# Optimization experiments

Measured on AMD Instinct MI355X. Metric: run time of the kernel, lower is better.

Reference implementation:

```python
import jax, jax.numpy as jnp
import numpy as np

NH, NOPE_D, ROPE_D, V_D, R = 16, 48, 16, 64, 128
EPS = 1e-6

def rms_norm(x, w):
    norm = jax.lax.rsqrt(jnp.mean(jnp.square(x), axis=-1, keepdims=True) + EPS)
    return x * norm * w

def apply_rope(x, cos, sin):
    # x: (..., rope_d); cos/sin broadcastable (..., rope_d//2)
    d = x.shape[-1]
    x1, x2 = x[..., : d // 2], x[..., d // 2 :]
    return jnp.concatenate([x1 * cos - x2 * sin, x2 * cos + x1 * sin], axis=-1)

def setup_inputs() -> dict:
    key = jax.random.key(0)
    ks = jax.random.split(key, 8)
    B, T, D = 2, 2048, 1024
    s = lambda fan_in: 1.0 / np.sqrt(fan_in)
    return {
        "x": jax.random.normal(ks[0], (B, T, D), jnp.float32),
        "cos": jax.random.uniform(ks[1], (T, ROPE_D // 2), jnp.float32),
        "sin": jax.random.uniform(ks[2], (T, ROPE_D // 2), jnp.float32),
        "Wq": jax.random.normal(ks[3], (NH * (NOPE_D + ROPE_D), D), jnp.float32) * s(D),
        "q_norm_w": jnp.ones((NOPE_D + ROPE_D,), jnp.float32),
        "Wkva": jax.random.normal(ks[4], (R + ROPE_D, D), jnp.float32) * s(D),
        "kva_norm_w": jnp.ones((R,), jnp.float32),
        "Wkvb": jax.random.normal(ks[5], (NH * (NOPE_D + V_D), R), jnp.float32) * s(R),
        "Wo": jax.random.normal(ks[6], (D, NH * V_D), jnp.float32) * s(NH * V_D),
    }

def reference(x, cos, sin, Wq, q_norm_w, Wkva, kva_norm_w, Wkvb, Wo):
    B, T, D = x.shape
    # Q path: project, per-head RMSNorm over (nope+rope) dims, split
    q = (x @ Wq.T).reshape(B, T, NH, NOPE_D + ROPE_D)
    q = rms_norm(q, q_norm_w)
    q_nope, q_rope = q[..., :NOPE_D], q[..., NOPE_D:]
    # Low-rank KV path
    kv_a = x @ Wkva.T  # (B,T,R+ROPE_D)
    kv_latent = rms_norm(kv_a[..., :R], kva_norm_w)
    k_rope_raw = kv_a[..., R:]  # (B,T,ROPE_D) shared across heads
    kv_b = (kv_latent @ Wkvb.T).reshape(B, T, NH, NOPE_D + V_D)
    k_nope, v = kv_b[..., :NOPE_D], kv_b[..., NOPE_D:]
    # Decoupled RoPE
    cos_t = cos[None, :T, None, :]  # (1,T,1,rope_d/2)
    sin_t = sin[None, :T, None, :]
    q_rope = apply_rope(q_rope, cos_t, sin_t)
    k_rope = apply_rope(k_rope_raw[:, :, None, :], cos[None, :T, None, :], sin[None, :T, None, :])
    k_rope = jnp.broadcast_to(k_rope, (B, T, NH, ROPE_D))
    q_full = jnp.concatenate([q_nope, q_rope], axis=-1)  # (B,T,NH,64)
    k_full = jnp.concatenate([k_nope, k_rope], axis=-1)
    # Causal attention, scale = 1/sqrt(nope+rope)
    scale = (NOPE_D + ROPE_D) ** -0.5
    scores = jnp.einsum("bqhd,bkhd->bhqk", q_full, k_full) * scale
    causal = jnp.tril(jnp.ones((T, T), bool))
    scores = jnp.where(causal[None, None], scores, -jnp.inf)
    attn = jax.nn.softmax(scores, axis=-1)
    out = jnp.einsum("bhqk,bkhd->bqhd", attn, v).reshape(B, T, NH * V_D)
    return out @ Wo.T
```

## Files before the change

### kernel.cpp

```cpp
#include <hip/hip_runtime.h>
#include <hip/hip_bf16.h>
#include <math.h>

#define NH 16
#define T_ 2048
#define B_ 2
#define D_ 1024
#define EPS 1e-6f

typedef __attribute__((ext_vector_type(8))) short bf16x8;
typedef __attribute__((ext_vector_type(4))) float f32x4;

__device__ __forceinline__ float wred_sum(float v){
  #pragma unroll
  for (int o = 32; o > 0; o >>= 1) v += __shfl_xor(v, o, 64);
  return v;
}

__device__ __forceinline__ unsigned pack_bf16(float a, float b){
  __hip_bfloat162 t = __float22bfloat162_rn(make_float2(a, b));
  unsigned r; __builtin_memcpy(&r, &t, 4); return r;
}

__device__ __forceinline__ void gload_lds16(const void* g, void* l){
  __builtin_amdgcn_global_load_lds((const __attribute__((address_space(1))) void*)g,
                                   (__attribute__((address_space(3))) void*)l, 16, 0, 0);
}

__global__ __launch_bounds__(256)
void cvt5(const float* __restrict__ x, const float* __restrict__ wq,
          const float* __restrict__ wkva, const float* __restrict__ wkvb,
          const float* __restrict__ wo,
          __hip_bfloat16* __restrict__ xb, __hip_bfloat16* __restrict__ wqb,
          __hip_bfloat16* __restrict__ wkvab, __hip_bfloat16* __restrict__ wkvbb,
          __hip_bfloat16* __restrict__ wob)
{
  const int i = blockIdx.x * 256 + threadIdx.x;
  const float* s; __hip_bfloat16* d; size_t soff, doff;
  if      (i < 1048576) { s = x;    d = xb;    soff = doff = i; }
  else if (i < 1310720) { s = wq;   d = wqb;   soff = doff = i - 1048576; }
  else if (i < 1347584) { s = wkva; d = wkvab; soff = doff = i - 1310720; }
  else if (i < 1404928) {
    const int off = i - 1347584;
    const int srow = off >> 5, c4 = off & 31;
    const int h = srow / 112, dd = srow % 112;
    const int drow = (dd < 48) ? (h*48 + dd) : (768 + h*64 + (dd - 48));
    s = wkvb; d = wkvbb; soff = off; doff = (size_t)drow*32 + c4;
  }
  else                  { s = wo;   d = wob;   soff = doff = i - 1404928; }
  float4 v = *(const float4*)(s + soff * 4);
  *(__hip_bfloat162*)(d + doff * 4)     = __float22bfloat162_rn(make_float2(v.x, v.y));
  *(__hip_bfloat162*)(d + doff * 4 + 2) = __float22bfloat162_rn(make_float2(v.z, v.w));
}

template<typename CT>
__global__ __launch_bounds__(256, 2)
void gemm_bt64(const __hip_bfloat16* __restrict__ A, const __hip_bfloat16* __restrict__ W,
               CT* __restrict__ C, int M, int N, int K)
{
  __shared__ __hip_bfloat16 As[2][128 * 64];
  __shared__ __hip_bfloat16 Ws[2][64 * 64];
  const int tid = threadIdx.x;
  const int wv = tid >> 6, lane = tid & 63;
  const int m = lane & 15, quad = lane >> 4;
  const int bm = blockIdx.y * 128, bn = blockIdx.x * 64;

  const __hip_bfloat16* ga[4];
  const __hip_bfloat16* gw[2];
  #pragma unroll
  for (int i = 0; i < 4; i++) {
    const int slot = i*256 + tid;
    const int row = slot >> 3, cb = slot & 7;
    ga[i] = A + (size_t)(bm + row) * K + ((cb ^ (row & 7)) << 3);
  }
  #pragma unroll
  for (int i = 0; i < 2; i++) {
    const int slot = i*256 + tid;
    const int row = slot >> 3, cb = slot & 7;
    int wr = bn + row; if (wr >= N) wr = N - 1;
    gw[i] = W + (size_t)wr * K + ((cb ^ (row & 7)) << 3);
  }
  auto stage = [&](int buf){
    #pragma unroll
    for (int i = 0; i < 4; i++) { gload_lds16(ga[i], &As[buf][(i*256 + wv*64)*8]); ga[i] += 64; }
    #pragma unroll
    for (int i = 0; i < 2; i++) { gload_lds16(gw[i], &Ws[buf][(i*256 + wv*64)*8]); gw[i] += 64; }
  };

  f32x4 acc[2][4];
  #pragma unroll
  for (int mi = 0; mi < 2; mi++)
    #pragma unroll
    for (int nj = 0; nj < 4; nj++) acc[mi][nj] = (f32x4){0.f,0.f,0.f,0.f};

  stage(0);
  const int iters = K >> 6;
  for (int it = 0; it < iters; it++) {
    const int cur = it & 1;
    __syncthreads();
    if (it + 1 < iters) stage(cur ^ 1);
    #pragma unroll
    for (int ks = 0; ks < 2; ks++) {
      const int cb = ((ks*4 + quad) ^ (m & 7)) << 3;
      bf16x8 af[2], wf[4];
      #pragma unroll
      for (int mi = 0; mi < 2; mi++)
        af[mi] = *(const bf16x8*)(&As[cur][(wv*32 + mi*16 + m) * 64 + cb]);
      #pragma unroll
      for (int nj = 0; nj < 4; nj++)
        wf[nj] = *(const bf16x8*)(&Ws[cur][(nj*16 + m) * 64 + cb]);
      #pragma unroll
      for (int mi = 0; mi < 2; mi++)
        #pragma unroll
        for (int nj = 0; nj < 4; nj++)
          acc[mi][nj] = __builtin_amdgcn_mfma_f32_16x16x32_bf16(af[mi], wf[nj], acc[mi][nj], 0, 0, 0);
    }
  }

  #pragma unroll
  for (int mi = 0; mi < 2; mi++)
    #pragma unroll
    for (int nj = 0; nj < 4; nj++) {
      const int col = bn + nj*16 + m;
      if (col < N) {
        #pragma unroll
        for (int r = 0; r < 4; r++) {
          const int row = bm + wv*32 + mi*16 + quad*4 + r;
          if constexpr (sizeof(CT) == 2)
            C[(size_t)row * N + col] = (CT)__float2bfloat16(acc[mi][nj][r]);
          else
            C[(size_t)row * N + col] = acc[mi][nj][r];
        }
      }
    }
}

__global__ __launch_bounds__(256, 2)
void gemm_qkva(const __hip_bfloat16* __restrict__ A, const __hip_bfloat16* __restrict__ Wqb,
               const __hip_bfloat16* __restrict__ Wkvab,
               const float* __restrict__ qw, const float* __restrict__ cosp,
               const float* __restrict__ sinp,
               __hip_bfloat16* __restrict__ qb, float* __restrict__ kva)
{
  __shared__ __hip_bfloat16 As[2][128 * 64];
  __shared__ __hip_bfloat16 Ws[2][64 * 64];
  const int K = 1024;
  const int tid = threadIdx.x;
  const int wv = tid >> 6, lane = tid & 63;
  const int m = lane & 15, quad = lane >> 4;
  const int bm = blockIdx.y * 128;
  const bool isq = blockIdx.x < 16;
  const __hip_bfloat16* W = isq ? Wqb : Wkvab;
  const int bn = isq ? blockIdx.x*64 : (blockIdx.x - 16)*64;
  const int Nw = isq ? 1024 : 144;

  const __hip_bfloat16* ga[4];
  const __hip_bfloat16* gw[2];
  #pragma unroll
  for (int i = 0; i < 4; i++) {
    const int slot = i*256 + tid;
    const int row = slot >> 3, cb = slot & 7;
    ga[i] = A + (size_t)(bm + row) * K + ((cb ^ (row & 7)) << 3);
  }
  #pragma unroll
  for (int i = 0; i < 2; i++) {
    const int slot = i*256 + tid;
    const int row = slot >> 3, cb = slot & 7;
    int wr = bn + row; if (wr >= Nw) wr = Nw - 1;
    gw[i] = W + (size_t)wr * K + ((cb ^ (row & 7)) << 3);
  }
  auto stage = [&](int buf){
    #pragma unroll
    for (int i = 0; i < 4; i++) { gload_lds16(ga[i], &As[buf][(i*256 + wv*64)*8]); ga[i] += 64; }
    #pragma unroll
    for (int i = 0; i < 2; i++) { gload_lds16(gw[i], &Ws[buf][(i*256 + wv*64)*8]); gw[i] += 64; }
  };

  f32x4 acc[2][4];
  #pragma unroll
  for (int mi = 0; mi < 2; mi++)
    #pragma unroll
    for (int nj = 0; nj < 4; nj++) acc[mi][nj] = (f32x4){0.f,0.f,0.f,0.f};

  stage(0);
  for (int it = 0; it < 16; it++) {
    const int cur = it & 1;
    __syncthreads();
    if (it < 15) stage(cur ^ 1);
    #pragma unroll
    for (int ks = 0; ks < 2; ks++) {
      const int cb = ((ks*4 + quad) ^ (m & 7)) << 3;
      bf16x8 af[2], wf[4];
      #pragma unroll
      for (int mi = 0; mi < 2; mi++)
        af[mi] = *(const bf16x8*)(&As[cur][(wv*32 + mi*16 + m) * 64 + cb]);
      #pragma unroll
      for (int nj = 0; nj < 4; nj++)
        wf[nj] = *(const bf16x8*)(&Ws[cur][(nj*16 + m) * 64 + cb]);
      #pragma unroll
      for (int mi = 0; mi < 2; mi++)
        #pragma unroll
        for (int nj = 0; nj < 4; nj++)
          acc[mi][nj] = __builtin_amdgcn_mfma_f32_16x16x32_bf16(af[mi], wf[nj], acc[mi][nj], 0, 0, 0);
    }
  }

  if (isq) {
    const int head = blockIdx.x;
    float qwv[4];
    #pragma unroll
    for (int nj = 0; nj < 4; nj++) qwv[nj] = qw[nj*16 + m];
    const int j = m & 7;
    const float qscale = 0.125f * 1.44269504f;
    #pragma unroll
    for (int mi = 0; mi < 2; mi++) {
      #pragma unroll
      for (int r = 0; r < 4; r++) {
        float ss = 0.f;
        #pragma unroll
        for (int nj = 0; nj < 4; nj++) { const float t = acc[mi][nj][r]; ss = fmaf(t, t, ss); }
        ss += __shfl_xor(ss, 1, 64); ss += __shfl_xor(ss, 2, 64);
        ss += __shfl_xor(ss, 4, 64); ss += __shfl_xor(ss, 8, 64);
        const float nrm = rsqrtf(ss * (1.0f/64.0f) + EPS);
        float v[4];
        #pragma unroll
        for (int nj = 0; nj < 4; nj++) v[nj] = acc[mi][nj][r] * nrm * qwv[nj];
        const int grow = bm + wv*32 + mi*16 + quad*4 + r;
        const int t = grow & (T_ - 1);
        const int b = grow >> 11;
        const float part = __shfl_xor(v[3], 8, 64);
        const float c = cosp[t*8 + j], sn = sinp[t*8 + j];
        v[3] = (m < 8) ? (v[3]*c - part*sn) : (v[3]*c + part*sn);
        __hip_bfloat16* dst = qb + ((size_t)(b*NH + head)*T_ + t)*64 + m;
        #pragma unroll
        for (int nj = 0; nj < 4; nj++) dst[nj*16] = __float2bfloat16(v[nj] * qscale);
      }
    }
  } else {
    #pragma unroll
    for (int mi = 0; mi < 2; mi++)
      #pragma unroll
      for (int nj = 0; nj < 4; nj++) {
        const int col = bn + nj*16 + m;
        if (col < 144) {
          #pragma unroll
          for (int r = 0; r < 4; r++) {
            const int row = bm + wv*32 + mi*16 + quad*4 + r;
            kva[(size_t)row * 144 + col] = acc[mi][nj][r];
          }
        }
      }
  }
}

__global__ void prep_kv(const float* __restrict__ kva, const float* __restrict__ kw,
                        const float* __restrict__ cosp, const float* __restrict__ sinp,
                        __hip_bfloat16* __restrict__ kvl16, __hip_bfloat16* __restrict__ krope16)
{
  const int tid = threadIdx.x;
  const int bt = blockIdx.x;
  const int t = bt % T_;
  const float* row = kva + (size_t)bt * 144;
  const float v = row[tid];
  float s = wred_sum(v * v);
  __shared__ float red[2];
  if ((tid & 63) == 0) red[tid >> 6] = s;
  __syncthreads();
  const float total = red[0] + red[1];
  const float norm = rsqrtf(total * (1.0f/128.0f) + EPS);
  kvl16[(size_t)bt * 128 + tid] = __float2bfloat16(v * norm * kw[tid]);
  if (tid < 16) {
    const int j = tid & 7;
    const float c = cosp[t*8 + j], sn = sinp[t*8 + j];
    const float x1 = row[128 + j], x2 = row[136 + j];
    krope16[(size_t)bt * 16 + tid] = __float2bfloat16((tid < 8) ? (x1 * c - x2 * sn)
                                                               : (x2 * c + x1 * sn));
  }
}

__global__ __launch_bounds__(256, 2)
void gemm_kvb(const __hip_bfloat16* __restrict__ A, const __hip_bfloat16* __restrict__ W,
              __hip_bfloat16* __restrict__ knope, __hip_bfloat16* __restrict__ vt)
{
  __shared__ __hip_bfloat16 As[2][128 * 64];
  __shared__ __hip_bfloat16 Ws[2][64 * 64];
  const int K = 128;
  const int tid = threadIdx.x;
  const int wv = tid >> 6, lane = tid & 63;
  const int m = lane & 15, quad = lane >> 4;
  const int bm = blockIdx.y * 128, bn = blockIdx.x * 64;

  const __hip_bfloat16* ga[4];
  const __hip_bfloat16* gw[2];
  #pragma unroll
  for (int i = 0; i < 4; i++) {
    const int slot = i*256 + tid;
    const int row = slot >> 3, cb = slot & 7;
    ga[i] = A + (size_t)(bm + row) * K + ((cb ^ (row & 7)) << 3);
  }
  #pragma unroll
  for (int i = 0; i < 2; i++) {
    const int slot = i*256 + tid;
    const int row = slot >> 3, cb = slot & 7;
    gw[i] = W + (size_t)(bn + row) * K + ((cb ^ (row & 7)) << 3);
  }
  auto stage = [&](int buf){
    #pragma unroll
    for (int i = 0; i < 4; i++) { gload_lds16(ga[i], &As[buf][(i*256 + wv*64)*8]); ga[i] += 64; }
    #pragma unroll
    for (int i = 0; i < 2; i++) { gload_lds16(gw[i], &Ws[buf][(i*256 + wv*64)*8]); gw[i] += 64; }
  };

  f32x4 acc[2][4];
  #pragma unroll
  for (int mi = 0; mi < 2; mi++)
    #pragma unroll
    for (int nj = 0; nj < 4; nj++) acc[mi][nj] = (f32x4){0.f,0.f,0.f,0.f};

  stage(0);
  for (int it = 0; it < 2; it++) {
    const int cur = it & 1;
    __syncthreads();
    if (it == 0) stage(1);
    #pragma unroll
    for (int ks = 0; ks < 2; ks++) {
      const int cb = ((ks*4 + quad) ^ (m & 7)) << 3;
      bf16x8 af[2], wf[4];
      #pragma unroll
      for (int mi = 0; mi < 2; mi++)
        af[mi] = *(const bf16x8*)(&As[cur][(wv*32 + mi*16 + m) * 64 + cb]);
      #pragma unroll
      for (int nj = 0; nj < 4; nj++)
        wf[nj] = *(const bf16x8*)(&Ws[cur][(nj*16 + m) * 64 + cb]);
      #pragma unroll
      for (int mi = 0; mi < 2; mi++)
        #pragma unroll
        for (int nj = 0; nj < 4; nj++)
          acc[mi][nj] = __builtin_amdgcn_mfma_f32_16x16x32_bf16(af[mi], wf[nj], acc[mi][nj], 0, 0, 0);
    }
  }

  if (bn < 768) {
    #pragma unroll
    for (int mi = 0; mi < 2; mi++)
      #pragma unroll
      for (int nj = 0; nj < 4; nj++) {
        const int col = bn + nj*16 + m;
        #pragma unroll
        for (int r = 0; r < 4; r++) {
          const int row = bm + wv*32 + mi*16 + quad*4 + r;
          knope[(size_t)row * 768 + col] = __float2bfloat16(acc[mi][nj][r]);
        }
      }
  } else {
    __syncthreads();
    short* TL = (short*)&As[0][0];
    #pragma unroll
    for (int mi = 0; mi < 2; mi++)
      #pragma unroll
      for (int nj = 0; nj < 4; nj++) {
        const int d = nj*16 + m;
        #pragma unroll
        for (int r = 0; r < 4; r++) {
          const int tl = wv*32 + mi*16 + quad*4 + r;
          __hip_bfloat16 hv = __float2bfloat16(acc[mi][nj][r]);
          short sv; __builtin_memcpy(&sv, &hv, 2);
          TL[d*136 + tl] = sv;
        }
      }
    __syncthreads();
    const int h = (bn - 768) >> 6;
    const int b = bm >> 11;
    const int t0 = bm & (T_ - 1);
    #pragma unroll
    for (int i = 0; i < 4; i++) {
      const int unit = i*256 + tid;
      const int d = unit >> 4, tu = unit & 15;
      *(bf16x8*)(vt + ((size_t)(b*NH + h)*64 + d)*T_ + t0 + tu*8)
          = *(const bf16x8*)(TL + d*136 + tu*8);
    }
  }
}

__device__ __forceinline__ void fa_softmax_fixed(f32x4 (&s)[8], const bool diag,
    const int k0, const int qglob, const int m, const int quad,
    float& lrun, bf16x8 (&a)[4])
{
  if (diag) {
    #pragma unroll
    for (int sub = 0; sub < 8; sub++)
      #pragma unroll
      for (int r = 0; r < 4; r++)
        if (k0 + sub*16 + quad*4 + r > qglob) s[sub][r] = -1e30f;
  }
  float p[8][4];
  #pragma unroll
  for (int sub = 0; sub < 8; sub++)
    #pragma unroll
    for (int r = 0; r < 4; r++) {
      const float e = exp2f(s[sub][r] - 48.0f);
      p[sub][r] = e; lrun += e;
    }

  unsigned u[8][2];
  #pragma unroll
  for (int sub = 0; sub < 8; sub++) {
    u[sub][0] = pack_bf16(p[sub][0], p[sub][1]);
    u[sub][1] = pack_bf16(p[sub][2], p[sub][3]);
  }
  #pragma unroll
  for (int c = 0; c < 4; c++) {
    union { int i[4]; bf16x8 v; } au;
    #pragma unroll
    for (int w4 = 0; w4 < 4; w4++) {
      const int src = (((2*quad + (w4 >> 1)) & 3) << 4) | m;
      const int lo = __shfl((int)u[c*2][w4 & 1], src, 64);
      const int hi = __shfl((int)u[c*2+1][w4 & 1], src, 64);
      au.i[w4] = (quad & 2) ? hi : lo;
    }
    a[c] = au.v;
  }
}

__device__ __forceinline__ void fa_store(float lrun, f32x4 (&oacc)[4],
    const int b, const int qrow0, const int h, const int m, const int quad,
    __hip_bfloat16* __restrict__ aout)
{
  lrun += __shfl_xor(lrun, 16, 64);
  lrun += __shfl_xor(lrun, 32, 64);
  float lr[4];
  #pragma unroll
  for (int r = 0; r < 4; r++) lr[r] = __shfl(lrun, (quad << 2) | r, 64);
  #pragma unroll
  for (int vs = 0; vs < 4; vs++)
    #pragma unroll
    for (int r = 0; r < 4; r++)
      aout[(size_t)(b*T_ + qrow0 + quad*4 + r) * 1024 + h*64 + vs*16 + m]
          = __float2bfloat16(oacc[vs][r] / lr[r]);
}

__global__ __launch_bounds__(256, 2)
void attn_pair2(const __hip_bfloat16* __restrict__ qb,
                const __hip_bfloat16* __restrict__ knope,
                const __hip_bfloat16* __restrict__ krope16,
                const __hip_bfloat16* __restrict__ vt16,
                __hip_bfloat16* __restrict__ aout)
{
  __shared__ __hip_bfloat16 SL[32768];
  const int tid = threadIdx.x;
  const int wv = tid >> 6, lane = tid & 63;
  const int m = lane & 15, quad = lane >> 4;
  const int ta = blockIdx.x;
  const int tb = 31 - ta;
  const int bh = blockIdx.y;
  const int b = bh >> 4, h = bh & 15;
  const int qbaseA = ta*64 + wv*16;
  const int qbaseB = tb*64 + wv*16;
  const int ntA = (ta + 2) >> 1;
  const int ntB = (tb + 2) >> 1;

  const __hip_bfloat16* qra = qb + ((size_t)bh*T_ + qbaseA + m)*64 + quad*8;
  const bf16x8 qA0 = *(const bf16x8*)qra, qA1 = *(const bf16x8*)(qra + 32);
  const __hip_bfloat16* qrb = qb + ((size_t)bh*T_ + qbaseB + m)*64 + quad*8;
  const bf16x8 qB0 = *(const bf16x8*)qrb, qB1 = *(const bf16x8*)(qrb + 32);

  const __hip_bfloat16* pK[4]; size_t iK[4];
  const __hip_bfloat16* pV[4];
  #pragma unroll
  for (int i = 0; i < 4; i++) {
    const int slot = i*256 + tid;
    const int krow = slot >> 3;
    const int kde = (slot & 7) ^ (krow & 7);
    if (kde < 6) { pK[i] = knope + (size_t)(b*T_ + krow)*768 + h*48 + kde*8; iK[i] = (size_t)128*768; }
    else         { pK[i] = krope16 + (size_t)(b*T_ + krow)*16 + (kde-6)*8;   iK[i] = (size_t)128*16; }
    const int vd = slot >> 4;
    const int vde = (slot & 15) ^ (vd & 7);
    pV[i] = vt16 + ((size_t)bh*64 + vd)*T_ + vde*8;
  }

  auto stage = [&](int buf){
    #pragma unroll
    for (int i = 0; i < 4; i++) {
      gload_lds16(pK[i], SL + buf*8192 + (i*256 + wv*64)*8);
      gload_lds16(pV[i], SL + 16384 + buf*8192 + (i*256 + wv*64)*8);
      pK[i] += iK[i]; pV[i] += 128;
    }
  };

  f32x4 oA[4], oB[4];
  #pragma unroll
  for (int vs = 0; vs < 4; vs++) { oA[vs] = (f32x4){0.f,0.f,0.f,0.f}; oB[vs] = (f32x4){0.f,0.f,0.f,0.f}; }
  float lA = 0.f, lB = 0.f;

  const int sw0 = quad ^ (m & 7);
  stage(0);

  for (int kt = 0; kt < ntB; kt++) {
    const int cur = kt & 1;
    __syncthreads();
    const __hip_bfloat16* Kc = SL + cur*8192;
    const __hip_bfloat16* Vc = SL + 16384 + cur*8192;
    const bool doA = (kt < ntA);

    f32x4 sA[8], sB[8];
    #pragma unroll
    for (int sub = 0; sub < 8; sub++) {
      const bf16x8 kf0 = *(const bf16x8*)(Kc + (sub*16 + m)*64 + sw0*8);
      const bf16x8 kf1 = *(const bf16x8*)(Kc + (sub*16 + m)*64 + (sw0^4)*8);
      f32x4 z = (f32x4){0.f,0.f,0.f,0.f};
      z = __builtin_amdgcn_mfma_f32_16x16x32_bf16(kf0, qB0, z, 0, 0, 0);
      z = __builtin_amdgcn_mfma_f32_16x16x32_bf16(kf1, qB1, z, 0, 0, 0);
      sB[sub] = z;
      if (doA) {
        f32x4 y = (f32x4){0.f,0.f,0.f,0.f};
        y = __builtin_amdgcn_mfma_f32_16x16x32_bf16(kf0, qA0, y, 0, 0, 0);
        y = __builtin_amdgcn_mfma_f32_16x16x32_bf16(kf1, qA1, y, 0, 0, 0);
        sA[sub] = y;
      }
    }

    if (kt + 1 < ntB) stage(cur ^ 1);

    bf16x8 aA[4], aB[4];
    fa_softmax_fixed(sB, kt == ntB-1, kt*128, qbaseB + m, m, quad, lB, aB);
    if (doA) fa_softmax_fixed(sA, kt == ntA-1, kt*128, qbaseA + m, m, quad, lA, aA);

    #pragma unroll
    for (int vs = 0; vs < 4; vs++) {
      #pragma unroll
      for (int c = 0; c < 4; c++) {
        const bf16x8 vf = *(const bf16x8*)(Vc + (vs*16 + m)*128 + (((c*4 + quad) ^ (m & 7)) << 3));
        oB[vs] = __builtin_amdgcn_mfma_f32_16x16x32_bf16(aB[c], vf, oB[vs], 0, 0, 0);
        if (doA) oA[vs] = __builtin_amdgcn_mfma_f32_16x16x32_bf16(aA[c], vf, oA[vs], 0, 0, 0);
      }
    }
  }

  fa_store(lA, oA, b, qbaseA, h, m, quad, aout);
  fa_store(lB, oB, b, qbaseB, h, m, quad, aout);
}

extern "C" void kernel_launch(void* const* d_in, const int* in_sizes, int n_in,
                              void* d_out, int out_size, void* d_ws, size_t ws_size,
                              hipStream_t stream)
{
  const float* x    = (const float*)d_in[0];
  const float* cosp = (const float*)d_in[1];
  const float* sinp = (const float*)d_in[2];
  const float* Wq   = (const float*)d_in[3];
  const float* qw   = (const float*)d_in[4];
  const float* Wkva = (const float*)d_in[5];
  const float* kw   = (const float*)d_in[6];
  const float* Wkvb = (const float*)d_in[7];
  const float* Wo   = (const float*)d_in[8];
  float* out = (float*)d_out;

  float* kva = (float*)d_ws;
  __hip_bfloat16* xb16    = (__hip_bfloat16*)(kva + 589824);
  __hip_bfloat16* knope16 = xb16 + 4194304;
  __hip_bfloat16* kvl16   = knope16 + 3145728;
  __hip_bfloat16* qb16    = kvl16 + 524288;
  __hip_bfloat16* vt16    = qb16 + 4194304;
  __hip_bfloat16* krope16 = vt16 + 4194304;
  __hip_bfloat16* Wqb     = krope16 + 65536;
  __hip_bfloat16* Wkvab   = Wqb + 1048576;
  __hip_bfloat16* Wkvbb   = Wkvab + 147456;
  __hip_bfloat16* Wob     = Wkvbb + 229376;
  __hip_bfloat16* ab16    = Wob + 1048576;

  const int M = B_ * T_;

  cvt5<<<6512, 256, 0, stream>>>(x, Wq, Wkva, Wkvb, Wo, xb16, Wqb, Wkvab, Wkvbb, Wob);
  gemm_qkva<<<dim3(19, 32), 256, 0, stream>>>(xb16, Wqb, Wkvab, qw, cosp, sinp, qb16, kva);
  prep_kv<<<M, 128, 0, stream>>>(kva, kw, cosp, sinp, kvl16, krope16);
  gemm_kvb<<<dim3(28, 32), 256, 0, stream>>>(kvl16, Wkvbb, knope16, vt16);
  attn_pair2<<<dim3(16, B_ * NH), 256, 0, stream>>>(qb16, knope16, krope16, vt16, ab16);
  gemm_bt64<float><<<dim3(16, 32), 256, 0, stream>>>(ab16, Wob, out, M, 1024, 1024);
}
```

Baseline: 185.1 us.

## Replace paired-tile attention with single 64-key tiles and diagonal skip

The attention kernel no longer pairs two 64-row query tiles per block over 128-key steps. It now gives each block one query tile and walks 64-key tiles, skipping the masked QK MFMAs on the diagonal tile. Blocks are permuted across query tiles to balance the causal load, and LDS is halved so four blocks can fit per CU. The cost is that K/V are no longer shared between two query tiles, and there are twice as many blocks and barriers per key.

```diff
diff --git a/kernel.cpp b/kernel.cpp
--- a/kernel.cpp
+++ b/kernel.cpp
@@ -382,46 +382,6 @@
   }
 }
 
-__device__ __forceinline__ void fa_softmax_fixed(f32x4 (&s)[8], const bool diag,
-    const int k0, const int qglob, const int m, const int quad,
-    float& lrun, bf16x8 (&a)[4])
-{
-  if (diag) {
-    #pragma unroll
-    for (int sub = 0; sub < 8; sub++)
-      #pragma unroll
-      for (int r = 0; r < 4; r++)
-        if (k0 + sub*16 + quad*4 + r > qglob) s[sub][r] = -1e30f;
-  }
-  float p[8][4];
-  #pragma unroll
-  for (int sub = 0; sub < 8; sub++)
-    #pragma unroll
-    for (int r = 0; r < 4; r++) {
-      const float e = exp2f(s[sub][r] - 48.0f);
-      p[sub][r] = e; lrun += e;
-    }
-
-  unsigned u[8][2];
-  #pragma unroll
-  for (int sub = 0; sub < 8; sub++) {
-    u[sub][0] = pack_bf16(p[sub][0], p[sub][1]);
-    u[sub][1] = pack_bf16(p[sub][2], p[sub][3]);
-  }
-  #pragma unroll
-  for (int c = 0; c < 4; c++) {
-    union { int i[4]; bf16x8 v; } au;
-    #pragma unroll
-    for (int w4 = 0; w4 < 4; w4++) {
-      const int src = (((2*quad + (w4 >> 1)) & 3) << 4) | m;
-      const int lo = __shfl((int)u[c*2][w4 & 1], src, 64);
-      const int hi = __shfl((int)u[c*2+1][w4 & 1], src, 64);
-      au.i[w4] = (quad & 2) ? hi : lo;
-    }
-    a[c] = au.v;
-  }
-}
-
 __device__ __forceinline__ void fa_store(float lrun, f32x4 (&oacc)[4],
     const int b, const int qrow0, const int h, const int m, const int quad,
     __hip_bfloat16* __restrict__ aout)
@@ -439,105 +399,131 @@
           = __float2bfloat16(oacc[vs][r] / lr[r]);
 }
 
-__global__ __launch_bounds__(256, 2)
-void attn_pair2(const __hip_bfloat16* __restrict__ qb,
-                const __hip_bfloat16* __restrict__ knope,
-                const __hip_bfloat16* __restrict__ krope16,
-                const __hip_bfloat16* __restrict__ vt16,
-                __hip_bfloat16* __restrict__ aout)
-{
-  __shared__ __hip_bfloat16 SL[32768];
+__global__ __launch_bounds__(256, 4)
+void attn_tile(const __hip_bfloat16* __restrict__ qb,
+               const __hip_bfloat16* __restrict__ knope,
+               const __hip_bfloat16* __restrict__ krope16,
+               const __hip_bfloat16* __restrict__ vt16,
+               __hip_bfloat16* __restrict__ aout)
+{
+  __shared__ __hip_bfloat16 SL[16384];
   const int tid = threadIdx.x;
   const int wv = tid >> 6, lane = tid & 63;
   const int m = lane & 15, quad = lane >> 4;
-  const int ta = blockIdx.x;
-  const int tb = 31 - ta;
+  const int idx = (blockIdx.x + blockIdx.y) & 31;
+  const int pj = idx & 7, pk = idx >> 3;
+  const int qt = (pk == 0) ? pj : (pk == 1) ? (15 - pj) : (pk == 2) ? (16 + pj) : (31 - pj);
   const int bh = blockIdx.y;
   const int b = bh >> 4, h = bh & 15;
-  const int qbaseA = ta*64 + wv*16;
-  const int qbaseB = tb*64 + wv*16;
-  const int ntA = (ta + 2) >> 1;
-  const int ntB = (tb + 2) >> 1;
-
-  const __hip_bfloat16* qra = qb + ((size_t)bh*T_ + qbaseA + m)*64 + quad*8;
-  const bf16x8 qA0 = *(const bf16x8*)qra, qA1 = *(const bf16x8*)(qra + 32);
-  const __hip_bfloat16* qrb = qb + ((size_t)bh*T_ + qbaseB + m)*64 + quad*8;
-  const bf16x8 qB0 = *(const bf16x8*)qrb, qB1 = *(const bf16x8*)(qrb + 32);
-
-  const __hip_bfloat16* pK[4]; size_t iK[4];
-  const __hip_bfloat16* pV[4];
-  #pragma unroll
-  for (int i = 0; i < 4; i++) {
+  const int qbase = qt*64 + wv*16;
+  const int nt = qt + 1;
+
+  const __hip_bfloat16* qr = qb + ((size_t)bh*T_ + qbase + m)*64 + quad*8;
+  const bf16x8 q0 = *(const bf16x8*)qr, q1 = *(const bf16x8*)(qr + 32);
+
+  const __hip_bfloat16* pK[2]; size_t iK[2];
+  const __hip_bfloat16* pV[2];
+  #pragma unroll
+  for (int i = 0; i < 2; i++) {
     const int slot = i*256 + tid;
     const int krow = slot >> 3;
     const int kde = (slot & 7) ^ (krow & 7);
-    if (kde < 6) { pK[i] = knope + (size_t)(b*T_ + krow)*768 + h*48 + kde*8; iK[i] = (size_t)128*768; }
-    else         { pK[i] = krope16 + (size_t)(b*T_ + krow)*16 + (kde-6)*8;   iK[i] = (size_t)128*16; }
-    const int vd = slot >> 4;
-    const int vde = (slot & 15) ^ (vd & 7);
-    pV[i] = vt16 + ((size_t)bh*64 + vd)*T_ + vde*8;
+    if (kde < 6) { pK[i] = knope + (size_t)(b*T_ + krow)*768 + h*48 + kde*8; iK[i] = (size_t)64*768; }
+    else         { pK[i] = krope16 + (size_t)(b*T_ + krow)*16 + (kde-6)*8;   iK[i] = (size_t)64*16; }
+    pV[i] = vt16 + ((size_t)bh*64 + krow)*T_ + kde*8;
   }
 
   auto stage = [&](int buf){
     #pragma unroll
-    for (int i = 0; i < 4; i++) {
-      gload_lds16(pK[i], SL + buf*8192 + (i*256 + wv*64)*8);
-      gload_lds16(pV[i], SL + 16384 + buf*8192 + (i*256 + wv*64)*8);
-      pK[i] += iK[i]; pV[i] += 128;
+    for (int i = 0; i < 2; i++) {
+      gload_lds16(pK[i], SL + buf*4096 + (i*256 + wv*64)*8);
+      gload_lds16(pV[i], SL + 8192 + buf*4096 + (i*256 + wv*64)*8);
+      pK[i] += iK[i]; pV[i] += 64;
     }
   };
 
-  f32x4 oA[4], oB[4];
-  #pragma unroll
-  for (int vs = 0; vs < 4; vs++) { oA[vs] = (f32x4){0.f,0.f,0.f,0.f}; oB[vs] = (f32x4){0.f,0.f,0.f,0.f}; }
-  float lA = 0.f, lB = 0.f;
+  f32x4 o[4];
+  #pragma unroll
+  for (int vs = 0; vs < 4; vs++) o[vs] = (f32x4){0.f,0.f,0.f,0.f};
+  float lrun = 0.f;
 
   const int sw0 = quad ^ (m & 7);
   stage(0);
 
-  for (int kt = 0; kt < ntB; kt++) {
+  for (int kt = 0; kt < nt; kt++) {
     const int cur = kt & 1;
     __syncthreads();
-    const __hip_bfloat16* Kc = SL + cur*8192;
-    const __hip_bfloat16* Vc = SL + 16384 + cur*8192;
-    const bool doA = (kt < ntA);
-
-    f32x4 sA[8], sB[8];
-    #pragma unroll
-    for (int sub = 0; sub < 8; sub++) {
-      const bf16x8 kf0 = *(const bf16x8*)(Kc + (sub*16 + m)*64 + sw0*8);
-      const bf16x8 kf1 = *(const bf16x8*)(Kc + (sub*16 + m)*64 + (sw0^4)*8);
-      f32x4 z = (f32x4){0.f,0.f,0.f,0.f};
-      z = __builtin_amdgcn_mfma_f32_16x16x32_bf16(kf0, qB0, z, 0, 0, 0);
-      z = __builtin_amdgcn_mfma_f32_16x16x32_bf16(kf1, qB1, z, 0, 0, 0);
-      sB[sub] = z;
-      if (doA) {
-        f32x4 y = (f32x4){0.f,0.f,0.f,0.f};
-        y = __builtin_amdgcn_mfma_f32_16x16x32_bf16(kf0, qA0, y, 0, 0, 0);
-        y = __builtin_amdgcn_mfma_f32_16x16x32_bf16(kf1, qA1, y, 0, 0, 0);
-        sA[sub] = y;
-      }
-    }
-
-    if (kt + 1 < ntB) stage(cur ^ 1);
-
-    bf16x8 aA[4], aB[4];
-    fa_softmax_fixed(sB, kt == ntB-1, kt*128, qbaseB + m, m, quad, lB, aB);
-    if (doA) fa_softmax_fixed(sA, kt == ntA-1, kt*128, qbaseA + m, m, quad, lA, aA);
-
-    #pragma unroll
-    for (int vs = 0; vs < 4; vs++) {
-      #pragma unroll
-      for (int c = 0; c < 4; c++) {
-        const bf16x8 vf = *(const bf16x8*)(Vc + (vs*16 + m)*128 + (((c*4 + quad) ^ (m & 7)) << 3));
-        oB[vs] = __builtin_amdgcn_mfma_f32_16x16x32_bf16(aB[c], vf, oB[vs], 0, 0, 0);
-        if (doA) oA[vs] = __builtin_amdgcn_mfma_f32_16x16x32_bf16(aA[c], vf, oA[vs], 0, 0, 0);
-      }
-    }
-  }
-
-  fa_store(lA, oA, b, qbaseA, h, m, quad, aout);
-  fa_store(lB, oB, b, qbaseB, h, m, quad, aout);
+    const __hip_bfloat16* Kc = SL + cur*4096;
+    const __hip_bfloat16* Vc = SL + 8192 + cur*4096;
+    const bool dtile = (kt == qt);
+
+    f32x4 s[4];
+    #pragma unroll
+    for (int sub = 0; sub < 4; sub++) {
+      if (!dtile || sub <= wv) {
+        const bf16x8 kf0 = *(const bf16x8*)(Kc + (sub*16 + m)*64 + sw0*8);
+        const bf16x8 kf1 = *(const bf16x8*)(Kc + (sub*16 + m)*64 + (sw0^4)*8);
+        f32x4 z = (f32x4){0.f,0.f,0.f,0.f};
+        z = __builtin_amdgcn_mfma_f32_16x16x32_bf16(kf0, q0, z, 0, 0, 0);
+        z = __builtin_amdgcn_mfma_f32_16x16x32_bf16(kf1, q1, z, 0, 0, 0);
+        s[sub] = z;
+      } else {
+        s[sub] = (f32x4){-1e30f,-1e30f,-1e30f,-1e30f};
+      }
+    }
+
+    if (kt + 1 < nt) stage(cur ^ 1);
+
+    if (dtile) {
+      #pragma unroll
+      for (int sub = 0; sub < 4; sub++) {
+        if (sub == wv) {
+          #pragma unroll
+          for (int r = 0; r < 4; r++)
+            if (quad*4 + r > m) s[sub][r] = -1e30f;
+        }
+      }
+    }
+
+    float p[4][4];
+    #pragma unroll
+    for (int sub = 0; sub < 4; sub++)
+      #pragma unroll
+      for (int r = 0; r < 4; r++) {
+        const float e = exp2f(s[sub][r] - 48.0f);
+        p[sub][r] = e; lrun += e;
+      }
+
+    unsigned u[4][2];
+    #pragma unroll
+    for (int sub = 0; sub < 4; sub++) {
+      u[sub][0] = pack_bf16(p[sub][0], p[sub][1]);
+      u[sub][1] = pack_bf16(p[sub][2], p[sub][3]);
+    }
+    bf16x8 a[2];
+    #pragma unroll
+    for (int c = 0; c < 2; c++) {
+      union { int i[4]; bf16x8 v; } au;
+      #pragma unroll
+      for (int w4 = 0; w4 < 4; w4++) {
+        const int src = (((2*quad + (w4 >> 1)) & 3) << 4) | m;
+        const int lo = __shfl((int)u[c*2][w4 & 1], src, 64);
+        const int hi = __shfl((int)u[c*2+1][w4 & 1], src, 64);
+        au.i[w4] = (quad & 2) ? hi : lo;
+      }
+      a[c] = au.v;
+    }
+
+    #pragma unroll
+    for (int vs = 0; vs < 4; vs++)
+      #pragma unroll
+      for (int c = 0; c < 2; c++) {
+        const bf16x8 vf = *(const bf16x8*)(Vc + (vs*16 + m)*64 + (((c*4 + quad) ^ (m & 7)) << 3));
+        o[vs] = __builtin_amdgcn_mfma_f32_16x16x32_bf16(a[c], vf, o[vs], 0, 0, 0);
+      }
+  }
+
+  fa_store(lrun, o, b, qbase, h, m, quad, aout);
 }
 
 extern "C" void kernel_launch(void* const* d_in, const int* in_sizes, int n_in,
@@ -574,6 +560,6 @@
   gemm_qkva<<<dim3(19, 32), 256, 0, stream>>>(xb16, Wqb, Wkvab, qw, cosp, sinp, qb16, kva);
   prep_kv<<<M, 128, 0, stream>>>(kva, kw, cosp, sinp, kvl16, krope16);
   gemm_kvb<<<dim3(28, 32), 256, 0, stream>>>(kvl16, Wkvbb, knope16, vt16);
-  attn_pair2<<<dim3(16, B_ * NH), 256, 0, stream>>>(qb16, knope16, krope16, vt16, ab16);
+  attn_tile<<<dim3(32, B_ * NH), 256, 0, stream>>>(qb16, knope16, krope16, vt16, ab16);
   gemm_bt64<float><<<dim3(16, 32), 256, 0, stream>>>(ab16, Wob, out, M, 1024, 1024);
 }
```

Result: no change. 183.8 us (-0.7%).
